# Optimization experiments

Measured on AMD Instinct MI355X. Metric: run time of the kernel, lower is better.

Reference implementation:

```python
import jax, jax.numpy as jnp
import numpy as np

H = 8        # num_heads
D = 768      # d_model
DH = D // H  # d_head = 96


def setup_inputs() -> dict:
    key = jax.random.key(0)
    ks = jax.random.split(key, 12)
    B, S = 4, 2048
    s_in = 1.0 / np.sqrt(D)
    s_cat = 1.0 / np.sqrt(D)
    return {
        "input_querys": jax.random.normal(ks[0], (B, S, D), jnp.float32),
        "input_key": jax.random.normal(ks[1], (B, S, D), jnp.float32),
        "input_values": jax.random.normal(ks[2], (B, S, D), jnp.float32),
        # per-head projection weights, stacked over the head axis
        "Wq": jax.random.normal(ks[3], (H, D, DH), jnp.float32) * s_in,
        "bq": jax.random.normal(ks[4], (H, DH), jnp.float32) * s_in,
        "Wk": jax.random.normal(ks[5], (H, D, DH), jnp.float32) * s_in,
        "bk": jax.random.normal(ks[6], (H, DH), jnp.float32) * s_in,
        "Wv": jax.random.normal(ks[7], (H, D, DH), jnp.float32) * s_in,
        "bv": jax.random.normal(ks[8], (H, DH), jnp.float32) * s_in,
        # output linear: (H*DH) -> D
        "Wo": jax.random.normal(ks[9], (H * DH, D), jnp.float32) * s_cat,
        "bo": jax.random.normal(ks[10], (D,), jnp.float32) * s_cat,
    }


def reference(input_querys, input_key, input_values, Wq, bq, Wk, bk, Wv, bv, Wo, bo):
    # Per-head linear projections (vectorized over the head axis)
    # q/k/v: [B,S,D] -> [B,H,S,DH]
    Q = jnp.einsum("bsd,hdk->bhsk", input_querys, Wq) + bq[None, :, None, :]
    K = jnp.einsum("bsd,hdk->bhsk", input_key, Wk) + bk[None, :, None, :]
    V = jnp.einsum("bsd,hdk->bhsk", input_values, Wv) + bv[None, :, None, :]

    scale = 1.0 / jnp.sqrt(jnp.asarray(DH, Q.dtype))
    scores = jnp.einsum("bhsk,bhtk->bhst", Q, K) * scale  # [B,H,S,S]
    attn = jax.nn.softmax(scores, axis=-1)
    out = jnp.einsum("bhst,bhtk->bhsk", attn, V)  # [B,H,S,DH]

    # concat heads (head-major order matches torch.cat over ModuleList)
    B, _, S, _ = out.shape
    cat = out.transpose(0, 2, 1, 3).reshape(B, S, H * DH)
    return cat @ Wo + bo
```

## Files before the change

kernel.cpp:

```cpp
#include <hip/hip_runtime.h>


typedef unsigned short u16;
typedef _Float16 h16;
typedef h16 h16x8 __attribute__((ext_vector_type(8)));
typedef __fp16 fp16x2 __attribute__((ext_vector_type(2)));
typedef unsigned short u16x8 __attribute__((ext_vector_type(8)));
typedef unsigned short u16x4 __attribute__((ext_vector_type(4)));
typedef float f32x4 __attribute__((ext_vector_type(4)));

__device__ __forceinline__ u16 f2h(float f) {
  union { h16 h; u16 u; } c; c.h = (h16)f; return c.u;
}

__device__ __forceinline__ void gll16(const void* g, void* l) {
  __builtin_amdgcn_global_load_lds(
      (const __attribute__((address_space(1))) void*)g,
      (__attribute__((address_space(3))) void*)l, 16, 0, 0);
}

__global__ __launch_bounds__(256) void prep_kernel(
    const float* __restrict__ Wq, const float* __restrict__ Wk,
    const float* __restrict__ Wv, const float* __restrict__ Wo,
    const float* __restrict__ Xk, const float* __restrict__ Xv,
    u16* __restrict__ WqT, u16* __restrict__ WkT,
    u16* __restrict__ WvT, u16* __restrict__ WoT,
    u16* __restrict__ Xk16, u16* __restrict__ Xv16)
{
  const long gid = (long)blockIdx.x * 256 + threadIdx.x;
  if (gid >= 294912) {
    long i = gid - 294912;
    const int t = (i >= 786432) ? 1 : 0;
    const long e = (i - (long)t * 786432) * 8;
    const float* src = t ? Xv : Xk;
    u16* dst = t ? Xv16 : Xk16;
    f32x4 a = *(const f32x4*)(&src[e]);
    f32x4 b = *(const f32x4*)(&src[e + 4]);
    u16x8 v;
    #pragma unroll
    for (int j = 0; j < 4; j++) { v[j] = f2h(a[j]); v[4 + j] = f2h(b[j]); }
    *(u16x8*)(&dst[e]) = v;
    return;
  }
  int idx = (int)gid * 8;
  int region = idx / 589824;
  int i = idx % 589824;
  int n = i / 768;
  int d = i % 768;
  u16x8 v;
  if (region == 3) {
    #pragma unroll
    for (int j = 0; j < 8; j++) v[j] = f2h(Wo[(size_t)(d + j) * 768 + n]);
    *(u16x8*)(&WoT[i]) = v;
  } else {
    int h = n / 96, kk = n % 96;
    const float* W = (region == 0) ? Wq : (region == 1) ? Wk : Wv;
    u16* T = (region == 0) ? WqT : (region == 1) ? WkT : WvT;
    #pragma unroll
    for (int j = 0; j < 8; j++) v[j] = f2h(W[(size_t)h * 73728 + (size_t)(d + j) * 96 + kk]);
    *(u16x8*)(&T[i]) = v;
  }
}

#define GK 768

__global__ __launch_bounds__(256) void gemm_qkv(
    const float* __restrict__ Xq, const u16* __restrict__ Xk16,
    const u16* __restrict__ Xv16, const u16* __restrict__ WT,
    const float* __restrict__ bq, const float* __restrict__ bk,
    const float* __restrict__ bv,
    u16* __restrict__ Q16, u16* __restrict__ K16, u16* __restrict__ VT)
{
  const int z = blockIdx.z;
  const u16* BT = WT + (size_t)z * 589824;
  const float* bias = (z == 0) ? bq : (z == 1) ? bk : bv;

  __shared__ __align__(16) u16 As[128 * 32];
  __shared__ __align__(16) u16 Bs[64 * 32];
  const int tid = threadIdx.x;
  const int wave = tid >> 6;
  const int lane = tid & 63;
  const int quad = lane >> 4;
  const int l16 = lane & 15;
  const int m0 = blockIdx.x * 128;
  const int n0 = blockIdx.y * 64;

  f32x4 acc[2][4];
  #pragma unroll
  for (int i = 0; i < 2; i++)
    #pragma unroll
    for (int j = 0; j < 4; j++) acc[i][j] = (f32x4){0.f, 0.f, 0.f, 0.f};

  if (z == 0) {
    const float* A = Xq;
    const int ar = tid >> 2;
    const int ac = (tid & 3) * 8;

    f32x4 pf[4];
    u16x8 pb;
    {
      pf[0] = *(const f32x4*)(&A[(size_t)(m0 + ar) * GK + ac]);
      pf[1] = *(const f32x4*)(&A[(size_t)(m0 + ar) * GK + ac + 4]);
      pf[2] = *(const f32x4*)(&A[(size_t)(m0 + 64 + ar) * GK + ac]);
      pf[3] = *(const f32x4*)(&A[(size_t)(m0 + 64 + ar) * GK + ac + 4]);
      pb = *(const u16x8*)(&BT[(size_t)(n0 + ar) * GK + ac]);
    }

    for (int kt = 0; kt < 24; kt++) {
      u16x8 h0, h1;
      #pragma unroll
      for (int j = 0; j < 4; j++) {
        h0[j] = f2h(pf[0][j]); h0[4 + j] = f2h(pf[1][j]);
        h1[j] = f2h(pf[2][j]); h1[4 + j] = f2h(pf[3][j]);
      }
      *(u16x8*)(&As[ar * 32 + ac]) = h0;
      *(u16x8*)(&As[(64 + ar) * 32 + ac]) = h1;
      *(u16x8*)(&Bs[ar * 32 + ac]) = pb;
      __syncthreads();

      if (kt + 1 < 24) {
        const int k0 = (kt + 1) * 32;
        pf[0] = *(const f32x4*)(&A[(size_t)(m0 + ar) * GK + k0 + ac]);
        pf[1] = *(const f32x4*)(&A[(size_t)(m0 + ar) * GK + k0 + ac + 4]);
        pf[2] = *(const f32x4*)(&A[(size_t)(m0 + 64 + ar) * GK + k0 + ac]);
        pf[3] = *(const f32x4*)(&A[(size_t)(m0 + 64 + ar) * GK + k0 + ac + 4]);
        pb = *(const u16x8*)(&BT[(size_t)(n0 + ar) * GK + k0 + ac]);
      }

      h16x8 af[2], bf[4];
      #pragma unroll
      for (int mf = 0; mf < 2; mf++)
        af[mf] = *(const h16x8*)(&As[(wave * 32 + mf * 16 + l16) * 32 + quad * 8]);
      #pragma unroll
      for (int nf = 0; nf < 4; nf++)
        bf[nf] = *(const h16x8*)(&Bs[(nf * 16 + l16) * 32 + quad * 8]);
      #pragma unroll
      for (int mf = 0; mf < 2; mf++)
        #pragma unroll
        for (int nf = 0; nf < 4; nf++)
          acc[mf][nf] = __builtin_amdgcn_mfma_f32_16x16x32_f16(af[mf], bf[nf], acc[mf][nf], 0, 0, 0);

      if (kt + 1 < 24) __syncthreads();
    }
  } else {
    const u16* A = (z == 1) ? Xk16 : Xv16;
    const int Lr = lane >> 2, Lc = (lane & 3) * 8;
    const u16* gA0 = A + (size_t)(m0 + wave * 32 + Lr) * GK + Lc;
    const u16* gA1 = gA0 + (size_t)16 * GK;
    const u16* gB  = BT + (size_t)(n0 + wave * 16 + Lr) * GK + Lc;
    u16* lA0 = &As[(wave * 32) * 32];
    u16* lA1 = &As[(wave * 32 + 16) * 32];
    u16* lB  = &Bs[(wave * 16) * 32];

    for (int kt = 0; kt < 24; kt++) {
      gll16(gA0, lA0);
      gll16(gA1, lA1);
      gll16(gB, lB);
      gA0 += 32; gA1 += 32; gB += 32;
      __syncthreads();

      h16x8 af[2], bf[4];
      #pragma unroll
      for (int mf = 0; mf < 2; mf++)
        af[mf] = *(const h16x8*)(&As[(wave * 32 + mf * 16 + l16) * 32 + quad * 8]);
      #pragma unroll
      for (int nf = 0; nf < 4; nf++)
        bf[nf] = *(const h16x8*)(&Bs[(nf * 16 + l16) * 32 + quad * 8]);
      #pragma unroll
      for (int mf = 0; mf < 2; mf++)
        #pragma unroll
        for (int nf = 0; nf < 4; nf++)
          acc[mf][nf] = __builtin_amdgcn_mfma_f32_16x16x32_f16(af[mf], bf[nf], acc[mf][nf], 0, 0, 0);
      __syncthreads();
    }
  }

  u16* Yr = (z == 0) ? Q16 : K16;
  #pragma unroll
  for (int nf = 0; nf < 4; nf++) {
    const int n = n0 + nf * 16 + l16;
    const float bv2 = bias[n];
    #pragma unroll
    for (int mf = 0; mf < 2; mf++) {
      const int m = m0 + wave * 32 + mf * 16 + quad * 4;
      if (z == 2) {
        const int b = m >> 11, s = m & 2047;
        u16x4 pk;
        #pragma unroll
        for (int r = 0; r < 4; r++) pk[r] = f2h(acc[mf][nf][r] + bv2);
        *(u16x4*)(&VT[(size_t)b * 768 * 2048 + (size_t)n * 2048 + s]) = pk;
      } else {
        #pragma unroll
        for (int r = 0; r < 4; r++)
          Yr[(size_t)(m + r) * GK + n] = f2h(acc[mf][nf][r] + bv2);
      }
    }
  }
}

__global__ __launch_bounds__(256) void gemm_o(
    const u16* __restrict__ A, const u16* __restrict__ BT,
    const float* __restrict__ bias, float* __restrict__ Y)
{
  __shared__ __align__(16) u16 As[128 * 32];
  __shared__ __align__(16) u16 Bs[64 * 32];
  const int tid = threadIdx.x;
  const int wave = tid >> 6;
  const int lane = tid & 63;
  const int quad = lane >> 4;
  const int l16 = lane & 15;
  const int m0 = blockIdx.x * 128;
  const int n0 = blockIdx.y * 64;

  f32x4 acc[2][4];
  #pragma unroll
  for (int i = 0; i < 2; i++)
    #pragma unroll
    for (int j = 0; j < 4; j++) acc[i][j] = (f32x4){0.f, 0.f, 0.f, 0.f};

  const int Lr = lane >> 2, Lc = (lane & 3) * 8;
  const u16* gA0 = A + (size_t)(m0 + wave * 32 + Lr) * GK + Lc;
  const u16* gA1 = gA0 + (size_t)16 * GK;
  const u16* gB  = BT + (size_t)(n0 + wave * 16 + Lr) * GK + Lc;
  u16* lA0 = &As[(wave * 32) * 32];
  u16* lA1 = &As[(wave * 32 + 16) * 32];
  u16* lB  = &Bs[(wave * 16) * 32];

  for (int kt = 0; kt < 24; kt++) {
    gll16(gA0, lA0);
    gll16(gA1, lA1);
    gll16(gB, lB);
    gA0 += 32; gA1 += 32; gB += 32;
    __syncthreads();

    h16x8 af[2], bf[4];
    #pragma unroll
    for (int mf = 0; mf < 2; mf++)
      af[mf] = *(const h16x8*)(&As[(wave * 32 + mf * 16 + l16) * 32 + quad * 8]);
    #pragma unroll
    for (int nf = 0; nf < 4; nf++)
      bf[nf] = *(const h16x8*)(&Bs[(nf * 16 + l16) * 32 + quad * 8]);
    #pragma unroll
    for (int mf = 0; mf < 2; mf++)
      #pragma unroll
      for (int nf = 0; nf < 4; nf++)
        acc[mf][nf] = __builtin_amdgcn_mfma_f32_16x16x32_f16(af[mf], bf[nf], acc[mf][nf], 0, 0, 0);
    __syncthreads();
  }

  #pragma unroll
  for (int nf = 0; nf < 4; nf++) {
    const int n = n0 + nf * 16 + l16;
    const float bv = bias[n];
    #pragma unroll
    for (int mf = 0; mf < 2; mf++) {
      const int m = m0 + wave * 32 + mf * 16 + quad * 4;
      #pragma unroll
      for (int r = 0; r < 4; r++)
        Y[(size_t)(m + r) * GK + n] = acc[mf][nf][r] + bv;
    }
  }
}

#define SEQ 2048
#define LQK 104
#define LVT 72
#define LPS 72

__global__ __launch_bounds__(512, 4) void attn_kernel(
    const u16* __restrict__ Q, const u16* __restrict__ K,
    const u16* __restrict__ VT, u16* __restrict__ O)
{
  __shared__ __align__(16) u16 Ks[64 * LQK];
  __shared__ __align__(16) u16 Vt[96 * LVT];
  __shared__ __align__(16) u16 Ps[8][16 * LPS];

  const int tid = threadIdx.x;
  const int wave = tid >> 6;
  const int lane = tid & 63;
  const int quad = lane >> 4;
  const int l16 = lane & 15;

  const int bh = blockIdx.y;
  const int b = bh >> 3, h = bh & 7;
  const int q0 = blockIdx.x * 128;

  const size_t batch_off = (size_t)b * SEQ * 768;
  const u16* Kg = K + batch_off + h * 96;
  const u16* Vg = VT + (size_t)b * 768 * 2048 + (size_t)(h * 96) * 2048;

  h16x8 qf[3];
  {
    const u16* Qrow = Q + batch_off + (size_t)(q0 + wave * 16 + l16) * 768 + h * 96 + quad * 8;
    #pragma unroll
    for (int ks = 0; ks < 3; ks++) qf[ks] = *(const h16x8*)(&Qrow[ks * 32]);
  }

  const int kr0 = tid / 12, kc0 = (tid % 12) * 8;
  const int kr1 = (tid + 512) / 12, kc1 = ((tid + 512) % 12) * 8;
  const int vr0 = tid >> 3, vc0 = (tid & 7) * 8;
  const int vr1 = (tid + 512) >> 3, vc1 = ((tid + 512) & 7) * 8;
  const bool extra = tid < 256;

  f32x4 o[6];
  #pragma unroll
  for (int i = 0; i < 6; i++) o[i] = (f32x4){0.f, 0.f, 0.f, 0.f};
  float m_raw = -1e30f, lrow = 0.f;
  const float sc = 0.14724498f;

  u16* Pw = &Ps[wave][0];

  u16x8 kA, kB, vA, vB;
  kA = *(const u16x8*)(&Kg[(size_t)kr0 * 768 + kc0]);
  vA = *(const u16x8*)(&Vg[(size_t)vr0 * 2048 + vc0]);
  if (extra) {
    kB = *(const u16x8*)(&Kg[(size_t)kr1 * 768 + kc1]);
    vB = *(const u16x8*)(&Vg[(size_t)vr1 * 2048 + vc1]);
  }

  for (int kt = 0; kt < SEQ / 64; kt++) {
    *(u16x8*)(&Ks[kr0 * LQK + kc0]) = kA;
    *(u16x8*)(&Vt[vr0 * LVT + vc0]) = vA;
    if (extra) {
      *(u16x8*)(&Ks[kr1 * LQK + kc1]) = kB;
      *(u16x8*)(&Vt[vr1 * LVT + vc1]) = vB;
    }
    __syncthreads();

    if (kt + 1 < SEQ / 64) {
      const u16* Kn = Kg + (size_t)(kt + 1) * 64 * 768;
      const u16* Vn = Vg + (size_t)(kt + 1) * 64;
      kA = *(const u16x8*)(&Kn[(size_t)kr0 * 768 + kc0]);
      vA = *(const u16x8*)(&Vn[(size_t)vr0 * 2048 + vc0]);
      if (extra) {
        kB = *(const u16x8*)(&Kn[(size_t)kr1 * 768 + kc1]);
        vB = *(const u16x8*)(&Vn[(size_t)vr1 * 2048 + vc1]);
      }
    }

    f32x4 s[4];
    #pragma unroll
    for (int kf = 0; kf < 4; kf++) s[kf] = (f32x4){0.f, 0.f, 0.f, 0.f};
    __builtin_amdgcn_s_setprio(1);
    #pragma unroll
    for (int ks = 0; ks < 3; ks++) {
      #pragma unroll
      for (int kf = 0; kf < 4; kf++) {
        h16x8 a = *(const h16x8*)(&Ks[(kf * 16 + l16) * LQK + ks * 32 + quad * 8]);
        s[kf] = __builtin_amdgcn_mfma_f32_16x16x32_f16(a, qf[ks], s[kf], 0, 0, 0);
      }
    }
    __builtin_amdgcn_s_setprio(0);

    float mx = s[0][0];
    #pragma unroll
    for (int kf = 0; kf < 4; kf++)
      #pragma unroll
      for (int r = 0; r < 4; r++) mx = fmaxf(mx, s[kf][r]);
    mx = fmaxf(mx, __shfl_xor(mx, 16));
    mx = fmaxf(mx, __shfl_xor(mx, 32));
    if (__any(mx > m_raw + 54.0f)) {
      const float mnew = fmaxf(m_raw, mx);
      const float alpha = exp2f(sc * (m_raw - mnew));
      lrow *= alpha;
      #pragma unroll
      for (int nfo = 0; nfo < 6; nfo++)
        #pragma unroll
        for (int r = 0; r < 4; r++) o[nfo][r] *= alpha;
      m_raw = mnew;
    }
    const float c0 = sc * m_raw;
    float ps = 0.f;
    #pragma unroll
    for (int kf = 0; kf < 4; kf++)
      #pragma unroll
      for (int r = 0; r < 4; r++) {
        float p = exp2f(fmaf(s[kf][r], sc, -c0));
        s[kf][r] = p;
        ps += p;
      }
    lrow += ps;

    #pragma unroll
    for (int kf = 0; kf < 4; kf++)
      #pragma unroll
      for (int rp = 0; rp < 4; rp += 2) {
        fp16x2 pk = __builtin_amdgcn_cvt_pkrtz(s[kf][rp], s[kf][rp + 1]);
        *(fp16x2*)(&Pw[l16 * LPS + kf * 16 + quad * 4 + rp]) = pk;
      }

    __builtin_amdgcn_s_setprio(1);
    #pragma unroll
    for (int ks = 0; ks < 2; ks++) {
      h16x8 pfr = *(const h16x8*)(&Pw[l16 * LPS + ks * 32 + quad * 8]);
      #pragma unroll
      for (int nfo = 0; nfo < 6; nfo++) {
        h16x8 vfr = *(const h16x8*)(&Vt[(nfo * 16 + l16) * LVT + ks * 32 + quad * 8]);
        o[nfo] = __builtin_amdgcn_mfma_f32_16x16x32_f16(vfr, pfr, o[nfo], 0, 0, 0);
      }
    }
    __builtin_amdgcn_s_setprio(0);
    __syncthreads();
  }

  lrow += __shfl_xor(lrow, 16);
  lrow += __shfl_xor(lrow, 32);
  const float inv = 1.0f / lrow;
  u16* Ob = O + batch_off + (size_t)(q0 + wave * 16 + l16) * 768 + h * 96;
  #pragma unroll
  for (int nfo = 0; nfo < 6; nfo++) {
    fp16x2 lo = __builtin_amdgcn_cvt_pkrtz(o[nfo][0] * inv, o[nfo][1] * inv);
    fp16x2 hi = __builtin_amdgcn_cvt_pkrtz(o[nfo][2] * inv, o[nfo][3] * inv);
    *(fp16x2*)(&Ob[nfo * 16 + quad * 4]) = lo;
    *(fp16x2*)(&Ob[nfo * 16 + quad * 4 + 2]) = hi;
  }
}

extern "C" void kernel_launch(void* const* d_in, const int* in_sizes, int n_in,
                              void* d_out, int out_size, void* d_ws, size_t ws_size,
                              hipStream_t stream) {
  const float* Xq = (const float*)d_in[0];
  const float* Xk = (const float*)d_in[1];
  const float* Xv = (const float*)d_in[2];
  const float* Wq = (const float*)d_in[3];
  const float* bq = (const float*)d_in[4];
  const float* Wk = (const float*)d_in[5];
  const float* bk = (const float*)d_in[6];
  const float* Wv = (const float*)d_in[7];
  const float* bv = (const float*)d_in[8];
  const float* Wo = (const float*)d_in[9];
  const float* bo = (const float*)d_in[10];

  u16* wsu = (u16*)d_ws;
  u16* WT   = wsu;
  u16* WoT  = wsu + 3 * 589824;
  u16* Q16  = wsu + 4 * 589824;
  u16* Xk16 = Q16 + 6291456;
  u16* Xv16 = Xk16 + 6291456;

  u16* outu = (u16*)d_out;
  u16* VTb = outu;
  u16* K16 = outu + 6291456;

  u16* A16 = (u16*)d_in[0];

  prep_kernel<<<7296, 256, 0, stream>>>(Wq, Wk, Wv, Wo, Xk, Xv,
                                        WT, WT + 589824, WT + 2 * 589824, WoT,
                                        Xk16, Xv16);
  gemm_qkv<<<dim3(64, 12, 3), 256, 0, stream>>>(Xq, Xk16, Xv16, WT, bq, bk, bv, Q16, K16, VTb);
  attn_kernel<<<dim3(16, 32), 512, 0, stream>>>(Q16, K16, VTb, A16);
  gemm_o<<<dim3(64, 12), 256, 0, stream>>>(A16, WoT, bo, (float*)d_out);
}
```

Before: 299.9 us.

## Tile weight transposes via LDS, widen GEMM N-tiles, double-buffer attention K/V

The prep kernel now transposes weights through shared-memory tiles so reads and writes are coalesced, and it also converts Xq to fp16 so the Q projection uses the same global_load_lds path as K and V. Both GEMMs widen the N tile from 64 to 128, which improves operand reuse but halves the number of blocks and raises accumulator register use. The attention kernel double-buffers K and V in LDS, so the next tile's store and prefetch overlap compute and only one barrier is needed per step. The P stores are also packed into 4-wide writes. This adds an extra fp16 copy of Xq in workspace and raises LDS and register usage.

```diff
diff --git a/kernel.cpp b/kernel.cpp
--- a/kernel.cpp
+++ b/kernel.cpp
@@ -5,6 +5,7 @@
 typedef _Float16 h16;
 typedef h16 h16x8 __attribute__((ext_vector_type(8)));
 typedef __fp16 fp16x2 __attribute__((ext_vector_type(2)));
+typedef __fp16 fp16x4 __attribute__((ext_vector_type(4)));
 typedef unsigned short u16x8 __attribute__((ext_vector_type(8)));
 typedef unsigned short u16x4 __attribute__((ext_vector_type(4)));
 typedef float f32x4 __attribute__((ext_vector_type(4)));
@@ -23,17 +24,20 @@
     const float* __restrict__ Wq, const float* __restrict__ Wk,
     const float* __restrict__ Wv, const float* __restrict__ Wo,
     const float* __restrict__ Xk, const float* __restrict__ Xv,
+    const float* __restrict__ Xq,
     u16* __restrict__ WqT, u16* __restrict__ WkT,
     u16* __restrict__ WvT, u16* __restrict__ WoT,
-    u16* __restrict__ Xk16, u16* __restrict__ Xv16)
+    u16* __restrict__ Xk16, u16* __restrict__ Xv16, u16* __restrict__ Xq16)
 {
-  const long gid = (long)blockIdx.x * 256 + threadIdx.x;
-  if (gid >= 294912) {
-    long i = gid - 294912;
-    const int t = (i >= 786432) ? 1 : 0;
-    const long e = (i - (long)t * 786432) * 8;
-    const float* src = t ? Xv : Xk;
-    u16* dst = t ? Xv16 : Xk16;
+  const int bid = blockIdx.x;
+  const int tid = threadIdx.x;
+
+  if (bid >= 432) {
+    const int i = bid - 432;
+    const int t = i / 3072;
+    const long e = ((long)(i % 3072) * 256 + tid) * 8;
+    const float* src = (t == 0) ? Xk : (t == 1) ? Xv : Xq;
+    u16* dst = (t == 0) ? Xk16 : (t == 1) ? Xv16 : Xq16;
     f32x4 a = *(const f32x4*)(&src[e]);
     f32x4 b = *(const f32x4*)(&src[e + 4]);
     u16x8 v;
@@ -42,30 +46,62 @@
     *(u16x8*)(&dst[e]) = v;
     return;
   }
-  int idx = (int)gid * 8;
-  int region = idx / 589824;
-  int i = idx % 589824;
-  int n = i / 768;
-  int d = i % 768;
-  u16x8 v;
-  if (region == 3) {
-    #pragma unroll
-    for (int j = 0; j < 8; j++) v[j] = f2h(Wo[(size_t)(d + j) * 768 + n]);
-    *(u16x8*)(&WoT[i]) = v;
-  } else {
-    int h = n / 96, kk = n % 96;
-    const float* W = (region == 0) ? Wq : (region == 1) ? Wk : Wv;
-    u16* T = (region == 0) ? WqT : (region == 1) ? WkT : WvT;
-    #pragma unroll
-    for (int j = 0; j < 8; j++) v[j] = f2h(W[(size_t)h * 73728 + (size_t)(d + j) * 96 + kk]);
-    *(u16x8*)(&T[i]) = v;
+
+  if (bid < 288) {
+    __shared__ u16 Lt[96][72];
+    const int w = bid / 96;
+    const int r = bid % 96;
+    const int h = r / 12, dt = r % 12;
+    const float* W = (w == 0) ? Wq : (w == 1) ? Wk : Wv;
+    u16* T = (w == 0) ? WqT : (w == 1) ? WkT : WvT;
+    const float* src = W + (size_t)h * 73728 + (size_t)dt * 64 * 96;
+    #pragma unroll
+    for (int p = 0; p < 6; p++) {
+      const int lin = p * 1024 + tid * 4;
+      f32x4 v = *(const f32x4*)(&src[lin]);
+      const int d = lin / 96, kk = lin % 96;
+      #pragma unroll
+      for (int j = 0; j < 4; j++) Lt[kk + j][d] = f2h(v[j]);
+    }
+    __syncthreads();
+    #pragma unroll
+    for (int c = 0; c < 3; c++) {
+      const int ch = c * 256 + tid;
+      const int kk = ch >> 3, dc = ch & 7;
+      u16x8 o = *(const u16x8*)(&Lt[kk][dc * 8]);
+      *(u16x8*)(&T[(size_t)(h * 96 + kk) * 768 + dt * 64 + dc * 8]) = o;
+    }
+    return;
+  }
+
+  {
+    __shared__ u16 Lo[64][72];
+    const int i = bid - 288;
+    const int kt = i / 12, nt = i % 12;
+    const float* src = Wo + (size_t)(kt * 64) * 768 + nt * 64;
+    #pragma unroll
+    for (int p = 0; p < 4; p++) {
+      const int lin = p * 1024 + tid * 4;
+      const int kr = lin >> 6, nc = lin & 63;
+      f32x4 v = *(const f32x4*)(&src[(size_t)kr * 768 + nc]);
+      #pragma unroll
+      for (int j = 0; j < 4; j++) Lo[nc + j][kr] = f2h(v[j]);
+    }
+    __syncthreads();
+    #pragma unroll
+    for (int c = 0; c < 2; c++) {
+      const int ch = c * 256 + tid;
+      const int nr = ch >> 3, kc = ch & 7;
+      u16x8 o = *(const u16x8*)(&Lo[nr][kc * 8]);
+      *(u16x8*)(&WoT[(size_t)(nt * 64 + nr) * 768 + kt * 64 + kc * 8]) = o;
+    }
   }
 }
 
 #define GK 768
 
 __global__ __launch_bounds__(256) void gemm_qkv(
-    const float* __restrict__ Xq, const u16* __restrict__ Xk16,
+    const u16* __restrict__ Xq16, const u16* __restrict__ Xk16,
     const u16* __restrict__ Xv16, const u16* __restrict__ WT,
     const float* __restrict__ bq, const float* __restrict__ bk,
     const float* __restrict__ bv,
@@ -74,110 +110,60 @@
   const int z = blockIdx.z;
   const u16* BT = WT + (size_t)z * 589824;
   const float* bias = (z == 0) ? bq : (z == 1) ? bk : bv;
+  const u16* A = (z == 0) ? Xq16 : (z == 1) ? Xk16 : Xv16;
 
   __shared__ __align__(16) u16 As[128 * 32];
-  __shared__ __align__(16) u16 Bs[64 * 32];
+  __shared__ __align__(16) u16 Bs[128 * 32];
   const int tid = threadIdx.x;
   const int wave = tid >> 6;
   const int lane = tid & 63;
   const int quad = lane >> 4;
   const int l16 = lane & 15;
   const int m0 = blockIdx.x * 128;
-  const int n0 = blockIdx.y * 64;
-
-  f32x4 acc[2][4];
+  const int n0 = blockIdx.y * 128;
+
+  f32x4 acc[2][8];
   #pragma unroll
   for (int i = 0; i < 2; i++)
     #pragma unroll
-    for (int j = 0; j < 4; j++) acc[i][j] = (f32x4){0.f, 0.f, 0.f, 0.f};
-
-  if (z == 0) {
-    const float* A = Xq;
-    const int ar = tid >> 2;
-    const int ac = (tid & 3) * 8;
-
-    f32x4 pf[4];
-    u16x8 pb;
-    {
-      pf[0] = *(const f32x4*)(&A[(size_t)(m0 + ar) * GK + ac]);
-      pf[1] = *(const f32x4*)(&A[(size_t)(m0 + ar) * GK + ac + 4]);
-      pf[2] = *(const f32x4*)(&A[(size_t)(m0 + 64 + ar) * GK + ac]);
-      pf[3] = *(const f32x4*)(&A[(size_t)(m0 + 64 + ar) * GK + ac + 4]);
-      pb = *(const u16x8*)(&BT[(size_t)(n0 + ar) * GK + ac]);
-    }
-
-    for (int kt = 0; kt < 24; kt++) {
-      u16x8 h0, h1;
-      #pragma unroll
-      for (int j = 0; j < 4; j++) {
-        h0[j] = f2h(pf[0][j]); h0[4 + j] = f2h(pf[1][j]);
-        h1[j] = f2h(pf[2][j]); h1[4 + j] = f2h(pf[3][j]);
-      }
-      *(u16x8*)(&As[ar * 32 + ac]) = h0;
-      *(u16x8*)(&As[(64 + ar) * 32 + ac]) = h1;
-      *(u16x8*)(&Bs[ar * 32 + ac]) = pb;
-      __syncthreads();
-
-      if (kt + 1 < 24) {
-        const int k0 = (kt + 1) * 32;
-        pf[0] = *(const f32x4*)(&A[(size_t)(m0 + ar) * GK + k0 + ac]);
-        pf[1] = *(const f32x4*)(&A[(size_t)(m0 + ar) * GK + k0 + ac + 4]);
-        pf[2] = *(const f32x4*)(&A[(size_t)(m0 + 64 + ar) * GK + k0 + ac]);
-        pf[3] = *(const f32x4*)(&A[(size_t)(m0 + 64 + ar) * GK + k0 + ac + 4]);
-        pb = *(const u16x8*)(&BT[(size_t)(n0 + ar) * GK + k0 + ac]);
-      }
-
-      h16x8 af[2], bf[4];
-      #pragma unroll
-      for (int mf = 0; mf < 2; mf++)
-        af[mf] = *(const h16x8*)(&As[(wave * 32 + mf * 16 + l16) * 32 + quad * 8]);
-      #pragma unroll
-      for (int nf = 0; nf < 4; nf++)
-        bf[nf] = *(const h16x8*)(&Bs[(nf * 16 + l16) * 32 + quad * 8]);
-      #pragma unroll
-      for (int mf = 0; mf < 2; mf++)
-        #pragma unroll
-        for (int nf = 0; nf < 4; nf++)
-          acc[mf][nf] = __builtin_amdgcn_mfma_f32_16x16x32_f16(af[mf], bf[nf], acc[mf][nf], 0, 0, 0);
-
-      if (kt + 1 < 24) __syncthreads();
-    }
-  } else {
-    const u16* A = (z == 1) ? Xk16 : Xv16;
-    const int Lr = lane >> 2, Lc = (lane & 3) * 8;
-    const u16* gA0 = A + (size_t)(m0 + wave * 32 + Lr) * GK + Lc;
-    const u16* gA1 = gA0 + (size_t)16 * GK;
-    const u16* gB  = BT + (size_t)(n0 + wave * 16 + Lr) * GK + Lc;
-    u16* lA0 = &As[(wave * 32) * 32];
-    u16* lA1 = &As[(wave * 32 + 16) * 32];
-    u16* lB  = &Bs[(wave * 16) * 32];
-
-    for (int kt = 0; kt < 24; kt++) {
-      gll16(gA0, lA0);
-      gll16(gA1, lA1);
-      gll16(gB, lB);
-      gA0 += 32; gA1 += 32; gB += 32;
-      __syncthreads();
-
-      h16x8 af[2], bf[4];
-      #pragma unroll
-      for (int mf = 0; mf < 2; mf++)
-        af[mf] = *(const h16x8*)(&As[(wave * 32 + mf * 16 + l16) * 32 + quad * 8]);
-      #pragma unroll
-      for (int nf = 0; nf < 4; nf++)
-        bf[nf] = *(const h16x8*)(&Bs[(nf * 16 + l16) * 32 + quad * 8]);
-      #pragma unroll
-      for (int mf = 0; mf < 2; mf++)
-        #pragma unroll
-        for (int nf = 0; nf < 4; nf++)
-          acc[mf][nf] = __builtin_amdgcn_mfma_f32_16x16x32_f16(af[mf], bf[nf], acc[mf][nf], 0, 0, 0);
-      __syncthreads();
-    }
+    for (int j = 0; j < 8; j++) acc[i][j] = (f32x4){0.f, 0.f, 0.f, 0.f};
+
+  const int Lr = lane >> 2, Lc = (lane & 3) * 8;
+  const u16* gA0 = A + (size_t)(m0 + wave * 32 + Lr) * GK + Lc;
+  const u16* gA1 = gA0 + (size_t)16 * GK;
+  const u16* gB0 = BT + (size_t)(n0 + wave * 32 + Lr) * GK + Lc;
+  const u16* gB1 = gB0 + (size_t)16 * GK;
+  u16* lA0 = &As[(wave * 32) * 32];
+  u16* lA1 = &As[(wave * 32 + 16) * 32];
+  u16* lB0 = &Bs[(wave * 32) * 32];
+  u16* lB1 = &Bs[(wave * 32 + 16) * 32];
+
+  for (int kt = 0; kt < 24; kt++) {
+    gll16(gA0, lA0);
+    gll16(gA1, lA1);
+    gll16(gB0, lB0);
+    gll16(gB1, lB1);
+    gA0 += 32; gA1 += 32; gB0 += 32; gB1 += 32;
+    __syncthreads();
+
+    h16x8 af[2], bf[8];
+    #pragma unroll
+    for (int mf = 0; mf < 2; mf++)
+      af[mf] = *(const h16x8*)(&As[(wave * 32 + mf * 16 + l16) * 32 + quad * 8]);
+    #pragma unroll
+    for (int nf = 0; nf < 8; nf++)
+      bf[nf] = *(const h16x8*)(&Bs[(nf * 16 + l16) * 32 + quad * 8]);
+    #pragma unroll
+    for (int mf = 0; mf < 2; mf++)
+      #pragma unroll
+      for (int nf = 0; nf < 8; nf++)
+        acc[mf][nf] = __builtin_amdgcn_mfma_f32_16x16x32_f16(af[mf], bf[nf], acc[mf][nf], 0, 0, 0);
+    __syncthreads();
   }
 
   u16* Yr = (z == 0) ? Q16 : K16;
   #pragma unroll
-  for (int nf = 0; nf < 4; nf++) {
+  for (int nf = 0; nf < 8; nf++) {
     const int n = n0 + nf * 16 + l16;
     const float bv2 = bias[n];
     #pragma unroll
@@ -203,53 +189,56 @@
     const float* __restrict__ bias, float* __restrict__ Y)
 {
   __shared__ __align__(16) u16 As[128 * 32];
-  __shared__ __align__(16) u16 Bs[64 * 32];
+  __shared__ __align__(16) u16 Bs[128 * 32];
   const int tid = threadIdx.x;
   const int wave = tid >> 6;
   const int lane = tid & 63;
   const int quad = lane >> 4;
   const int l16 = lane & 15;
   const int m0 = blockIdx.x * 128;
-  const int n0 = blockIdx.y * 64;
-
-  f32x4 acc[2][4];
+  const int n0 = blockIdx.y * 128;
+
+  f32x4 acc[2][8];
   #pragma unroll
   for (int i = 0; i < 2; i++)
     #pragma unroll
-    for (int j = 0; j < 4; j++) acc[i][j] = (f32x4){0.f, 0.f, 0.f, 0.f};
+    for (int j = 0; j < 8; j++) acc[i][j] = (f32x4){0.f, 0.f, 0.f, 0.f};
 
   const int Lr = lane >> 2, Lc = (lane & 3) * 8;
   const u16* gA0 = A + (size_t)(m0 + wave * 32 + Lr) * GK + Lc;
   const u16* gA1 = gA0 + (size_t)16 * GK;
-  const u16* gB  = BT + (size_t)(n0 + wave * 16 + Lr) * GK + Lc;
+  const u16* gB0 = BT + (size_t)(n0 + wave * 32 + Lr) * GK + Lc;
+  const u16* gB1 = gB0 + (size_t)16 * GK;
   u16* lA0 = &As[(wave * 32) * 32];
   u16* lA1 = &As[(wave * 32 + 16) * 32];
-  u16* lB  = &Bs[(wave * 16) * 32];
+  u16* lB0 = &Bs[(wave * 32) * 32];
+  u16* lB1 = &Bs[(wave * 32 + 16) * 32];
 
   for (int kt = 0; kt < 24; kt++) {
     gll16(gA0, lA0);
     gll16(gA1, lA1);
-    gll16(gB, lB);
-    gA0 += 32; gA1 += 32; gB += 32;
-    __syncthreads();
-
-    h16x8 af[2], bf[4];
+    gll16(gB0, lB0);
+    gll16(gB1, lB1);
+    gA0 += 32; gA1 += 32; gB0 += 32; gB1 += 32;
+    __syncthreads();
+
+    h16x8 af[2], bf[8];
     #pragma unroll
     for (int mf = 0; mf < 2; mf++)
       af[mf] = *(const h16x8*)(&As[(wave * 32 + mf * 16 + l16) * 32 + quad * 8]);
     #pragma unroll
-    for (int nf = 0; nf < 4; nf++)
+    for (int nf = 0; nf < 8; nf++)
       bf[nf] = *(const h16x8*)(&Bs[(nf * 16 + l16) * 32 + quad * 8]);
     #pragma unroll
     for (int mf = 0; mf < 2; mf++)
       #pragma unroll
-      for (int nf = 0; nf < 4; nf++)
+      for (int nf = 0; nf < 8; nf++)
         acc[mf][nf] = __builtin_amdgcn_mfma_f32_16x16x32_f16(af[mf], bf[nf], acc[mf][nf], 0, 0, 0);
     __syncthreads();
   }
 
   #pragma unroll
-  for (int nf = 0; nf < 4; nf++) {
+  for (int nf = 0; nf < 8; nf++) {
     const int n = n0 + nf * 16 + l16;
     const float bv = bias[n];
     #pragma unroll
@@ -263,6 +252,7 @@
 }
 
 #define SEQ 2048
+#define NT 32
 #define LQK 104
 #define LVT 72
 #define LPS 72
@@ -271,8 +261,8 @@
     const u16* __restrict__ Q, const u16* __restrict__ K,
     const u16* __restrict__ VT, u16* __restrict__ O)
 {
-  __shared__ __align__(16) u16 Ks[64 * LQK];
-  __shared__ __align__(16) u16 Vt[96 * LVT];
+  __shared__ __align__(16) u16 Ks[2][64 * LQK];
+  __shared__ __align__(16) u16 Vt[2][96 * LVT];
   __shared__ __align__(16) u16 Ps[8][16 * LPS];
 
   const int tid = threadIdx.x;
@@ -317,26 +307,28 @@
     kB = *(const u16x8*)(&Kg[(size_t)kr1 * 768 + kc1]);
     vB = *(const u16x8*)(&Vg[(size_t)vr1 * 2048 + vc1]);
   }
-
-  for (int kt = 0; kt < SEQ / 64; kt++) {
-    *(u16x8*)(&Ks[kr0 * LQK + kc0]) = kA;
-    *(u16x8*)(&Vt[vr0 * LVT + vc0]) = vA;
+  *(u16x8*)(&Ks[0][kr0 * LQK + kc0]) = kA;
+  *(u16x8*)(&Vt[0][vr0 * LVT + vc0]) = vA;
+  if (extra) {
+    *(u16x8*)(&Ks[0][kr1 * LQK + kc1]) = kB;
+    *(u16x8*)(&Vt[0][vr1 * LVT + vc1]) = vB;
+  }
+  {
+    const u16* Kn = Kg + (size_t)64 * 768;
+    const u16* Vn = Vg + 64;
+    kA = *(const u16x8*)(&Kn[(size_t)kr0 * 768 + kc0]);
+    vA = *(const u16x8*)(&Vn[(size_t)vr0 * 2048 + vc0]);
     if (extra) {
-      *(u16x8*)(&Ks[kr1 * LQK + kc1]) = kB;
-      *(u16x8*)(&Vt[vr1 * LVT + vc1]) = vB;
-    }
-    __syncthreads();
-
-    if (kt + 1 < SEQ / 64) {
-      const u16* Kn = Kg + (size_t)(kt + 1) * 64 * 768;
-      const u16* Vn = Vg + (size_t)(kt + 1) * 64;
-      kA = *(const u16x8*)(&Kn[(size_t)kr0 * 768 + kc0]);
-      vA = *(const u16x8*)(&Vn[(size_t)vr0 * 2048 + vc0]);
-      if (extra) {
-        kB = *(const u16x8*)(&Kn[(size_t)kr1 * 768 + kc1]);
-        vB = *(const u16x8*)(&Vn[(size_t)vr1 * 2048 + vc1]);
-      }
-    }
+      kB = *(const u16x8*)(&Kn[(size_t)kr1 * 768 + kc1]);
+      vB = *(const u16x8*)(&Vn[(size_t)vr1 * 2048 + vc1]);
+    }
+  }
+  __syncthreads();
+
+  for (int kt = 0; kt < NT; kt++) {
+    const int cur = kt & 1;
+    const u16* Kc = &Ks[cur][0];
+    const u16* Vc = &Vt[cur][0];
 
     f32x4 s[4];
     #pragma unroll
@@ -346,7 +338,7 @@
     for (int ks = 0; ks < 3; ks++) {
       #pragma unroll
       for (int kf = 0; kf < 4; kf++) {
-        h16x8 a = *(const h16x8*)(&Ks[(kf * 16 + l16) * LQK + ks * 32 + quad * 8]);
+        h16x8 a = *(const h16x8*)(&Kc[(kf * 16 + l16) * LQK + ks * 32 + quad * 8]);
         s[kf] = __builtin_amdgcn_mfma_f32_16x16x32_f16(a, qf[ks], s[kf], 0, 0, 0);
       }
     }
@@ -382,12 +374,12 @@
     lrow += ps;
 
     #pragma unroll
-    for (int kf = 0; kf < 4; kf++)
-      #pragma unroll
-      for (int rp = 0; rp < 4; rp += 2) {
-        fp16x2 pk = __builtin_amdgcn_cvt_pkrtz(s[kf][rp], s[kf][rp + 1]);
-        *(fp16x2*)(&Pw[l16 * LPS + kf * 16 + quad * 4 + rp]) = pk;
-      }
+    for (int kf = 0; kf < 4; kf++) {
+      fp16x2 a2 = __builtin_amdgcn_cvt_pkrtz(s[kf][0], s[kf][1]);
+      fp16x2 b2 = __builtin_amdgcn_cvt_pkrtz(s[kf][2], s[kf][3]);
+      fp16x4 w4; w4[0] = a2[0]; w4[1] = a2[1]; w4[2] = b2[0]; w4[3] = b2[1];
+      *(fp16x4*)(&Pw[l16 * LPS + kf * 16 + quad * 4]) = w4;
+    }
 
     __builtin_amdgcn_s_setprio(1);
     #pragma unroll
@@ -395,12 +387,33 @@
       h16x8 pfr = *(const h16x8*)(&Pw[l16 * LPS + ks * 32 + quad * 8]);
       #pragma unroll
       for (int nfo = 0; nfo < 6; nfo++) {
-        h16x8 vfr = *(const h16x8*)(&Vt[(nfo * 16 + l16) * LVT + ks * 32 + quad * 8]);
+        h16x8 vfr = *(const h16x8*)(&Vc[(nfo * 16 + l16) * LVT + ks * 32 + quad * 8]);
         o[nfo] = __builtin_amdgcn_mfma_f32_16x16x32_f16(vfr, pfr, o[nfo], 0, 0, 0);
       }
     }
     __builtin_amdgcn_s_setprio(0);
-    __syncthreads();
+
+    if (kt + 1 < NT) {
+      u16* Kw = &Ks[cur ^ 1][0];
+      u16* Vw = &Vt[cur ^ 1][0];
+      *(u16x8*)(&Kw[kr0 * LQK + kc0]) = kA;
+      *(u16x8*)(&Vw[vr0 * LVT + vc0]) = vA;
+      if (extra) {
+        *(u16x8*)(&Kw[kr1 * LQK + kc1]) = kB;
+        *(u16x8*)(&Vw[vr1 * LVT + vc1]) = vB;
+      }
+      if (kt + 2 < NT) {
+        const u16* Kn = Kg + (size_t)(kt + 2) * 64 * 768;
+        const u16* Vn = Vg + (size_t)(kt + 2) * 64;
+        kA = *(const u16x8*)(&Kn[(size_t)kr0 * 768 + kc0]);
+        vA = *(const u16x8*)(&Vn[(size_t)vr0 * 2048 + vc0]);
+        if (extra) {
+          kB = *(const u16x8*)(&Kn[(size_t)kr1 * 768 + kc1]);
+          vB = *(const u16x8*)(&Vn[(size_t)vr1 * 2048 + vc1]);
+        }
+      }
+      __syncthreads();
+    }
   }
 
   lrow += __shfl_xor(lrow, 16);
@@ -437,6 +450,7 @@
   u16* Q16  = wsu + 4 * 589824;
   u16* Xk16 = Q16 + 6291456;
   u16* Xv16 = Xk16 + 6291456;
+  u16* Xq16 = Xv16 + 6291456;
 
   u16* outu = (u16*)d_out;
   u16* VTb = outu;
@@ -444,10 +458,11 @@
 
   u16* A16 = (u16*)d_in[0];
 
-  prep_kernel<<<7296, 256, 0, stream>>>(Wq, Wk, Wv, Wo, Xk, Xv,
-                                        WT, WT + 589824, WT + 2 * 589824, WoT,
-                                        Xk16, Xv16);
-  gemm_qkv<<<dim3(64, 12, 3), 256, 0, stream>>>(Xq, Xk16, Xv16, WT, bq, bk, bv, Q16, K16, VTb);
+  prep_kernel<<<9648, 256, 0, stream>>>(
+      Wq, Wk, Wv, Wo, Xk, Xv, Xq,
+      WT, WT + 589824, WT + 2 * 589824, WoT, Xk16, Xv16, Xq16);
+  gemm_qkv<<<dim3(64, 6, 3), 256, 0, stream>>>(
+      Xq16, Xk16, Xv16, WT, bq, bk, bv, Q16, K16, VTb);
   attn_kernel<<<dim3(16, 32), 512, 0, stream>>>(Q16, K16, VTb, A16);
-  gemm_o<<<dim3(64, 12), 256, 0, stream>>>(A16, WoT, bo, (float*)d_out);
-}
+  gemm_o<<<dim3(64, 6), 256, 0, stream>>>(A16, WoT, bo, (float*)d_out);
+}
```

Measured after the change: 291.8 us. 2.7% less time.
